# Kernel optimization log

Hardware: AMD Instinct MI355X
Metric: run time of the kernel (lower is better)

The kernel has to match this reference:

```python
import jax, jax.numpy as jnp
import numpy as np

QUERY_LEVELS = jnp.array([300, 500, 900, 1500], dtype=jnp.int32)
MAX_K = 1500
NUM_BOUNDARIES = 3
MAX_OBJECTS = 1500
SCALE = MAX_OBJECTS / NUM_BOUNDARIES * 0.3  # 150.0


def _layernorm(x, g, b, eps=1e-5):
    m = jnp.mean(x, axis=-1, keepdims=True)
    v = jnp.var(x, axis=-1, keepdims=True)
    return (x - m) * jax.lax.rsqrt(v + eps) * g + b


def setup_inputs() -> dict:
    key = jax.random.key(0)
    ks = jax.random.split(key, 14)
    B, C, H, W = 8, 256, 100, 100
    s = 0.02
    return {
        "density_feature": jax.random.normal(ks[0], (B, C, H, W), jnp.float32),
        "encoder_features": jax.random.normal(ks[1], (B, C, H, W), jnp.float32),
        # input_norm (LayerNorm over 2*C)
        "ln_in_g": jnp.ones((2 * C,), jnp.float32),
        "ln_in_b": jnp.zeros((2 * C,), jnp.float32),
        # fc_boundary: Linear(2C->C), Linear(C->3)
        "fcb_w1": jax.random.normal(ks[2], (C, 2 * C), jnp.float32) * s,
        "fcb_b1": jnp.zeros((C,), jnp.float32),
        "fcb_w2": jax.random.normal(ks[3], (NUM_BOUNDARIES, C), jnp.float32) * s,
        "fcb_b2": jnp.full((NUM_BOUNDARIES,), -3.0, jnp.float32),
        "cr_ln_g": jnp.ones((C,), jnp.float32),
        "cr_ln_b": jnp.zeros((C,), jnp.float32),
        "cr_w1": jax.random.normal(ks[4], (C, C), jnp.float32) * s,
        "cr_b1": jnp.zeros((C,), jnp.float32),
        "cr_w2": jax.random.normal(ks[5], (1, C), jnp.float32) * s,
        "cr_b2": jnp.full((1,), 4.0, jnp.float32),
        # channel attention 1x1 convs: C->C//16->C
        "ca_w1": jax.random.normal(ks[6], (C // 16, C), jnp.float32) * s,
        "ca_b1": jnp.zeros((C // 16,), jnp.float32),
        "ca_w2": jax.random.normal(ks[7], (C, C // 16), jnp.float32) * s,
        "ca_b2": jnp.zeros((C,), jnp.float32),
        # spatial attention 7x7 conv, 2->1, no bias
        "sa_w": jax.random.normal(ks[8], (1, 2, 7, 7), jnp.float32) * s,
        # spatial_weight_conv 1x1, C->1
        "sw_w": jax.random.normal(ks[9], (1, C), jnp.float32) * s,
        "sw_b": jnp.zeros((1,), jnp.float32),
    }


def reference(density_feature, encoder_features, ln_in_g, ln_in_b,
              fcb_w1, fcb_b1, fcb_w2, fcb_b2,
              cr_ln_g, cr_ln_b, cr_w1, cr_b1, cr_w2, cr_b2,
              ca_w1, ca_b1, ca_w2, ca_b2, sa_w, sw_w, sw_b):
    B, C, H, W = density_feature.shape
    df = jnp.clip(density_feature, -5.0, 5.0)
    ef = jnp.clip(encoder_features, -5.0, 5.0)

    # ---- boundary prediction from density feature ----
    feat_avg = jnp.mean(df, axis=(2, 3))            # [B, C]
    feat_max = jnp.max(df, axis=(2, 3))             # [B, C]
    gfeat = jnp.concatenate([feat_avg, feat_max], axis=1)  # [B, 2C]
    gfeat = _layernorm(gfeat, ln_in_g, ln_in_b)
    h = jax.nn.relu(gfeat @ fcb_w1.T + fcb_b1)
    raw_boundaries = h @ fcb_w2.T + fcb_b2           # [B, 3]
    # cumulative: b_i = sum_{j<=i} (softplus(raw_j)*SCALE + 5)
    boundaries = jnp.cumsum(jax.nn.softplus(raw_boundaries) * SCALE + 5.0, axis=1)

    cr = _layernorm(feat_avg, cr_ln_g, cr_ln_b)
    cr = jax.nn.relu(cr @ cr_w1.T + cr_b1)
    pred_count = jax.nn.softplus(cr @ cr_w2.T + cr_b2)[:, 0]  # [B]

    # ---- num_queries via boundary comparison (eval: N_eval = pred_count) ----
    level = ((pred_count > boundaries[:, 0]).astype(jnp.int32)
             + (pred_count > boundaries[:, 1]).astype(jnp.int32)
             + (pred_count > boundaries[:, 2]).astype(jnp.int32))
    num_queries = QUERY_LEVELS[level]

    # ---- CBAM channel attention ----
    x = ef
    gap = jnp.mean(x, axis=(2, 3))                   # [B, C]
    ca = jax.nn.relu(gap @ ca_w1.T + ca_b1)
    ca = jax.nn.sigmoid(ca @ ca_w2.T + ca_b2)        # [B, C]
    x = x * ca[:, :, None, None]

    # ---- CBAM spatial attention ----
    sa_avg = jnp.mean(x, axis=1, keepdims=True)      # [B,1,H,W]
    sa_max = jnp.max(x, axis=1, keepdims=True)
    sa = jnp.concatenate([sa_avg, sa_max], axis=1)   # [B,2,H,W]
    sa = jax.lax.conv_general_dilated(sa, sa_w, (1, 1), [(3, 3), (3, 3)],
                                      dimension_numbers=("NCHW", "OIHW", "NCHW"))
    x = x * jax.nn.sigmoid(sa)

    # ---- spatial weight map + topk reference points ----
    wmap = jax.nn.sigmoid(jnp.einsum("bchw,oc->bohw", x, sw_w) + sw_b[None, :, None, None])
    spatial_weight_map = wmap.reshape(B, 1, H * W)
    weight_flat = wmap.reshape(B, H * W)
    actual_k = min(H * W, MAX_K)
    _, topk_ind = jax.lax.top_k(weight_flat, actual_k)   # [B, k]
    topk_y = ((topk_ind // W).astype(jnp.float32) + 0.5) / H
    topk_x = ((topk_ind % W).astype(jnp.float32) + 0.5) / W
    ref_points = jnp.stack([topk_x, topk_y], axis=-1)    # [B,k,2]
    ref_points = jnp.concatenate([ref_points, jnp.full_like(ref_points, 0.05)], axis=-1)
    if actual_k < MAX_K:
        pad = jnp.zeros((B, MAX_K - actual_k, 4), ref_points.dtype)
        ref_points = jnp.concatenate([ref_points, pad], axis=1)

    return (boundaries, raw_boundaries, pred_count, num_queries,
            spatial_weight_map, ref_points)
```

## Files before the change

kernel.cpp:

```cpp
#include <hip/hip_runtime.h>
#include <cstdint>
#include <cstddef>

#define BB 8
#define CC 256
#define HH 100
#define WW 100
#define HW 10000
#define KTOP 1500
#define QB 64

#define WS_AVG   0
#define WS_MAX   2048
#define WS_GAP   4096
#define WS_CA    6144
#define WS_CASW  8192
#define WS_SW    10240
#define WS_SAVG  90240
#define WS_SMAX  170240
#define WS_SEL   250240
#define WS_AK    250248

#define O_BND 0
#define O_RAW 24
#define O_CNT 48
#define O_NQ  56
#define O_WMAP 64
#define O_REF 80064

__device__ __forceinline__ float clip5(float v){ return fminf(fmaxf(v, -5.f), 5.f); }
__device__ __forceinline__ float softplusf(float x){ return fmaxf(x, 0.f) + log1pf(expf(-fabsf(x))); }
__device__ __forceinline__ float sigmoidf(float x){ return 1.f / (1.f + expf(-x)); }

__device__ __forceinline__ float wsum(float v){
#pragma unroll
  for (int o = 32; o; o >>= 1) v += __shfl_down(v, o, 64);
  return v;
}
__device__ __forceinline__ float wmaxr(float v){
#pragma unroll
  for (int o = 32; o; o >>= 1) v = fmaxf(v, __shfl_down(v, o, 64));
  return v;
}

__device__ __forceinline__ float bsum256(float v, volatile float* red){
  v = wsum(v);
  int w = threadIdx.x >> 6;
  if ((threadIdx.x & 63) == 0) red[w] = v;
  __syncthreads();
  float r = (red[0] + red[1]) + (red[2] + red[3]);
  __syncthreads();
  return r;
}

__device__ __forceinline__ void acc1(const float4& v, float& s, float& m){
  float a = clip5(v.x), b = clip5(v.y), c = clip5(v.z), d = clip5(v.w);
  s += (a + b) + (c + d);
  m = fmaxf(m, fmaxf(fmaxf(a, b), fmaxf(c, d)));
}

__global__ __launch_bounds__(256) void k_reduce(const float* __restrict__ df,
                                                const float* __restrict__ ef,
                                                float* __restrict__ ws){
  int gw = blockIdx.x * 4 + (threadIdx.x >> 6);
  bool isDf = gw < 2048;
  int bc = isDf ? gw : gw - 2048;
  int lane = threadIdx.x & 63;
  const float4* __restrict__ src =
      reinterpret_cast<const float4*>((isDf ? df : ef) + (size_t)bc * HW);

  float s = 0.f, m = -1e30f;
  float4 A[8], Bv[8];

#pragma unroll
  for (int j = 0; j < 8; j++) A[j]  = src[64 * j + lane];
#pragma unroll
  for (int j = 0; j < 8; j++) Bv[j] = src[512 + 64 * j + lane];
#pragma unroll
  for (int j = 0; j < 8; j++) acc1(A[j], s, m);
#pragma unroll
  for (int j = 0; j < 8; j++) A[j]  = src[1024 + 64 * j + lane];
#pragma unroll
  for (int j = 0; j < 8; j++) acc1(Bv[j], s, m);
#pragma unroll
  for (int j = 0; j < 8; j++) Bv[j] = src[1536 + 64 * j + lane];
#pragma unroll
  for (int j = 0; j < 8; j++) acc1(A[j], s, m);
#pragma unroll
  for (int j = 0; j < 7; j++) A[j]  = src[2048 + 64 * j + lane];
  A[7] = src[(2496 + lane < 2500) ? (2496 + lane) : lane];
#pragma unroll
  for (int j = 0; j < 8; j++) acc1(Bv[j], s, m);
#pragma unroll
  for (int j = 0; j < 7; j++) acc1(A[j], s, m);
  if (lane < 4) acc1(A[7], s, m);

  s = wsum(s); m = wmaxr(m);
  if (lane == 0){
    if (isDf){ ws[WS_AVG + bc] = s * (1.f / HW); ws[WS_MAX + bc] = m; }
    else      { ws[WS_GAP + bc] = s * (1.f / HW); }
  }
}

__global__ __launch_bounds__(256) void k_head(float* __restrict__ ws,
    const float* __restrict__ ln_g, const float* __restrict__ ln_b,
    const float* __restrict__ fw1, const float* __restrict__ fb1,
    const float* __restrict__ fw2, const float* __restrict__ fb2,
    const float* __restrict__ crg, const float* __restrict__ crb,
    const float* __restrict__ cw1, const float* __restrict__ cb1,
    const float* __restrict__ cw2, const float* __restrict__ cb2,
    const float* __restrict__ caw1, const float* __restrict__ cab1,
    const float* __restrict__ caw2, const float* __restrict__ cab2,
    const float* __restrict__ sw_w, float* __restrict__ out){
  int b = blockIdx.x, t = threadIdx.x;
  __shared__ float red[4];
  __shared__ __align__(16) float gl[512];
  __shared__ __align__(16) float hl[256];
  __shared__ float rawl[3];
  __shared__ float bnd[3];
  __shared__ __align__(16) float al[16];

  float fa = ws[WS_AVG + b * CC + t];
  float fm = ws[WS_MAX + b * CC + t];

  float s  = bsum256(fa + fm, red);
  float s2 = bsum256(fa * fa + fm * fm, red);
  float mean = s * (1.f / 512.f);
  float var  = s2 * (1.f / 512.f) - mean * mean;
  float inv  = rsqrtf(var + 1e-5f);
  gl[t]       = (fa - mean) * inv * ln_g[t]       + ln_b[t];
  gl[t + 256] = (fm - mean) * inv * ln_g[t + 256] + ln_b[t + 256];
  __syncthreads();

  {
    const float4* __restrict__ glv = reinterpret_cast<const float4*>(gl);
    const float4* __restrict__ w1v = reinterpret_cast<const float4*>(fw1 + t * 512);
    float acc = fb1[t];
#pragma unroll 8
    for (int k = 0; k < 128; k++){
      float4 g = glv[k], w = w1v[k];
      acc += g.x * w.x + g.y * w.y + g.z * w.z + g.w * w.w;
    }
    hl[t] = fmaxf(acc, 0.f);
  }
  __syncthreads();
  if (t < 3){
    const float4* __restrict__ hv  = reinterpret_cast<const float4*>(hl);
    const float4* __restrict__ w2v = reinterpret_cast<const float4*>(fw2 + t * 256);
    float r = fb2[t];
#pragma unroll 8
    for (int k = 0; k < 64; k++){
      float4 h = hv[k], w = w2v[k];
      r += h.x * w.x + h.y * w.y + h.z * w.z + h.w * w.w;
    }
    rawl[t] = r;
  }
  __syncthreads();
  if (t == 0){
    float cum = 0.f;
    for (int o = 0; o < 3; o++){
      float rv = rawl[o];
      out[O_RAW + b * 3 + o] = rv;
      cum += softplusf(rv) * 150.f + 5.f;
      out[O_BND + b * 3 + o] = cum;
      bnd[o] = cum;
    }
  }
  __syncthreads();

  float sc  = bsum256(fa, red);
  float sc2 = bsum256(fa * fa, red);
  float m2 = sc * (1.f / 256.f);
  float v2 = sc2 * (1.f / 256.f) - m2 * m2;
  float inv2 = rsqrtf(v2 + 1e-5f);
  hl[t] = (fa - m2) * inv2 * crg[t] + crb[t];
  __syncthreads();
  float h2;
  {
    const float4* __restrict__ hv  = reinterpret_cast<const float4*>(hl);
    const float4* __restrict__ w1v = reinterpret_cast<const float4*>(cw1 + t * 256);
    float acc2 = cb1[t];
#pragma unroll 8
    for (int k = 0; k < 64; k++){
      float4 h = hv[k], w = w1v[k];
      acc2 += h.x * w.x + h.y * w.y + h.z * w.z + h.w * w.w;
    }
    h2 = fmaxf(acc2, 0.f);
  }
  float pv = bsum256(h2 * cw2[t], red);
  if (t == 0){
    float pred = softplusf(pv + cb2[0]);
    out[O_CNT + b] = pred;
    int lvl = (pred > bnd[0]) + (pred > bnd[1]) + (pred > bnd[2]);
    const float QL[4] = {300.f, 500.f, 900.f, 1500.f};
    out[O_NQ + b] = QL[lvl];
  }

  float gp = ws[WS_GAP + b * CC + t];
  __syncthreads();
  hl[t] = gp;
  __syncthreads();
  if (t < 16){
    const float4* __restrict__ hv  = reinterpret_cast<const float4*>(hl);
    const float4* __restrict__ w1v = reinterpret_cast<const float4*>(caw1 + t * 256);
    float a = cab1[t];
#pragma unroll 8
    for (int k = 0; k < 64; k++){
      float4 h = hv[k], w = w1v[k];
      a += h.x * w.x + h.y * w.y + h.z * w.z + h.w * w.w;
    }
    al[t] = fmaxf(a, 0.f);
  }
  __syncthreads();
  float a2 = cab2[t];
  {
    const float4* __restrict__ av  = reinterpret_cast<const float4*>(al);
    const float4* __restrict__ w2v = reinterpret_cast<const float4*>(caw2 + t * 16);
#pragma unroll
    for (int k = 0; k < 4; k++){
      float4 h = av[k], w = w2v[k];
      a2 += h.x * w.x + h.y * w.y + h.z * w.z + h.w * w.w;
    }
  }
  float cav = sigmoidf(a2);
  ws[WS_CA + b * CC + t]   = cav;
  ws[WS_CASW + b * CC + t] = cav * sw_w[t];
}

__device__ __forceinline__ void px_acc(const float4& v, float ca, float cs,
                                       float4& sum, float4& mx, float4& sw){
  float a = clip5(v.x), b = clip5(v.y), c = clip5(v.z), d = clip5(v.w);
  sum.x += a * ca; sum.y += b * ca; sum.z += c * ca; sum.w += d * ca;
  mx.x = fmaxf(mx.x, a * ca); mx.y = fmaxf(mx.y, b * ca);
  mx.z = fmaxf(mx.z, c * ca); mx.w = fmaxf(mx.w, d * ca);
  sw.x = fmaf(a, cs, sw.x); sw.y = fmaf(b, cs, sw.y);
  sw.z = fmaf(c, cs, sw.z); sw.w = fmaf(d, cs, sw.w);
}

__global__ __launch_bounds__(256) void k_pixel(const float* __restrict__ ef,
                                               float* __restrict__ ws){
  int b = blockIdx.y;
  int t = threadIdx.x;
  int w = t >> 6, lane = t & 63;
  __shared__ float caL[256], cswL[256];
  __shared__ float4 part[3][4][QB];
  caL[t]  = ws[WS_CA + b * CC + t];
  cswL[t] = ws[WS_CASW + b * CC + t];
  __syncthreads();

  int q = blockIdx.x * QB + lane;
  const size_t st = HW / 4;
  size_t off = (q < (int)st) ? (size_t)q : 0;
  const float4* __restrict__ base =
      reinterpret_cast<const float4*>(ef + (size_t)b * CC * HW) + off;
  int c0 = w * 64;

  float4 sum = {0.f, 0.f, 0.f, 0.f};
  float4 mx  = {-1e30f, -1e30f, -1e30f, -1e30f};
  float4 sw  = {0.f, 0.f, 0.f, 0.f};

  float4 A[8], Bv[8];
#pragma unroll
  for (int j = 0; j < 8; j++) A[j] = base[(size_t)(c0 + j) * st];
#pragma unroll
  for (int s = 0; s < 4; s++){
    int cA = c0 + (2 * s) * 8;
    int cB = c0 + (2 * s + 1) * 8;
#pragma unroll
    for (int j = 0; j < 8; j++) Bv[j] = base[(size_t)(cB + j) * st];
#pragma unroll
    for (int j = 0; j < 8; j++) px_acc(A[j], caL[cA + j], cswL[cA + j], sum, mx, sw);
    if (s < 3){
      int cN = c0 + (2 * s + 2) * 8;
#pragma unroll
      for (int j = 0; j < 8; j++) A[j] = base[(size_t)(cN + j) * st];
    }
#pragma unroll
    for (int j = 0; j < 8; j++) px_acc(Bv[j], caL[cB + j], cswL[cB + j], sum, mx, sw);
  }

  part[0][w][lane] = sum;
  part[1][w][lane] = mx;
  part[2][w][lane] = sw;
  __syncthreads();
  if (t < QB){
    float4 S = part[0][0][t], M = part[1][0][t], W4 = part[2][0][t];
#pragma unroll
    for (int wv = 1; wv < 4; wv++){
      float4 s1 = part[0][wv][t], m1 = part[1][wv][t], w1 = part[2][wv][t];
      S.x += s1.x; S.y += s1.y; S.z += s1.z; S.w += s1.w;
      M.x = fmaxf(M.x, m1.x); M.y = fmaxf(M.y, m1.y);
      M.z = fmaxf(M.z, m1.z); M.w = fmaxf(M.w, m1.w);
      W4.x += w1.x; W4.y += w1.y; W4.z += w1.z; W4.w += w1.w;
    }
    int q2 = blockIdx.x * QB + t;
    if (q2 < (int)st){
      float4 avg = {S.x * (1.f / 256.f), S.y * (1.f / 256.f),
                    S.z * (1.f / 256.f), S.w * (1.f / 256.f)};
      reinterpret_cast<float4*>(ws + WS_SAVG + (size_t)b * HW)[q2] = avg;
      reinterpret_cast<float4*>(ws + WS_SMAX + (size_t)b * HW)[q2] = M;
      reinterpret_cast<float4*>(ws + WS_SW   + (size_t)b * HW)[q2] = W4;
    }
  }
}

__global__ __launch_bounds__(256) void k_conv(const float* __restrict__ ws,
                                              const float* __restrict__ sa_w,
                                              const float* __restrict__ sw_b,
                                              float* __restrict__ out){
  __shared__ float wc[98];
  if (threadIdx.x < 98) wc[threadIdx.x] = sa_w[threadIdx.x];
  __syncthreads();
  int b = blockIdx.y;
  int p = blockIdx.x * 256 + threadIdx.x;
  if (p >= HW) return;
  int h = p / WW, w = p - h * WW;
  const float* s0 = ws + WS_SAVG + (size_t)b * HW;
  const float* s1 = ws + WS_SMAX + (size_t)b * HW;
  float acc = 0.f;
#pragma unroll
  for (int kh = 0; kh < 7; kh++){
    int hy = h + kh - 3;
    if (hy < 0 || hy >= HH) continue;
#pragma unroll
    for (int kw = 0; kw < 7; kw++){
      int wx = w + kw - 3;
      if (wx < 0 || wx >= WW) continue;
      int q = hy * WW + wx;
      acc += s0[q] * wc[kh * 7 + kw] + s1[q] * wc[49 + kh * 7 + kw];
    }
  }
  float wm = sigmoidf(ws[WS_SW + (size_t)b * HW + p] * sigmoidf(acc) + sw_b[0]);
  out[O_WMAP + (size_t)b * HW + p] = wm;
}

__global__ __launch_bounds__(1024) void k_select(const float* __restrict__ outw,
                                                 float* __restrict__ ws,
                                                 float* __restrict__ out){
  __shared__ unsigned long long red64[16];
  __shared__ unsigned red32[16];
  __shared__ unsigned slo, shi, sbc;
  __shared__ unsigned acnt, runbase;
  int b = blockIdx.x, t = threadIdx.x;
  int w = t >> 6, lane = t & 63;

  const float* src = outw + O_WMAP + (size_t)b * HW;
  unsigned rv[10];
#pragma unroll
  for (int j = 0; j < 10; j++){
    int i = t + j * 1024;
    rv[j] = (i < HW) ? __float_as_uint(src[i]) : 0u;
  }

  unsigned lo = 0u, hi = 0xFFFFFFFFu;
  while (lo < hi){
    unsigned span = hi - lo;
    unsigned q1 = lo + (span >> 2);
    unsigned q2 = lo + (span >> 1);
    unsigned q3 = lo + span - (span >> 2);
    unsigned long long pk = 0;
#pragma unroll
    for (int j = 0; j < 10; j++){
      unsigned v = rv[j];
      pk += (unsigned long long)(v > q1)
          + ((unsigned long long)(v > q2) << 16)
          + ((unsigned long long)(v > q3) << 32);
    }
#pragma unroll
    for (int o = 32; o; o >>= 1) pk += __shfl_down(pk, o, 64);
    if (lane == 0) red64[w] = pk;
    __syncthreads();
    if (t == 0){
      unsigned long long tot = 0;
#pragma unroll
      for (int q = 0; q < 16; q++) tot += red64[q];
      unsigned c1 = (unsigned)(tot & 0xFFFFu);
      unsigned c2 = (unsigned)((tot >> 16) & 0xFFFFu);
      unsigned c3 = (unsigned)((tot >> 32) & 0xFFFFu);
      unsigned nlo, nhi;
      if (c1 < (unsigned)KTOP)      { nlo = lo;      nhi = q1; }
      else if (c2 < (unsigned)KTOP) { nlo = q1 + 1u; nhi = q2; }
      else if (c3 < (unsigned)KTOP) { nlo = q2 + 1u; nhi = q3; }
      else                          { nlo = q3 + 1u; nhi = hi; }
      slo = nlo; shi = nhi;
    }
    __syncthreads();
    lo = slo; hi = shi;
    __syncthreads();
  }
  unsigned vthr = lo;

  {
    unsigned c = 0;
#pragma unroll
    for (int j = 0; j < 10; j++) c += (rv[j] > vthr) ? 1u : 0u;
#pragma unroll
    for (int o = 32; o; o >>= 1) c += __shfl_down((int)c, o, 64);
    if (lane == 0) red32[w] = c;
    __syncthreads();
    if (t == 0){
      unsigned tot = 0;
#pragma unroll
      for (int q = 0; q < 16; q++) tot += red32[q];
      sbc = tot;
      acnt = 0; runbase = 0;
    }
    __syncthreads();
  }
  unsigned nabove = sbc;
  int neq = KTOP - (int)nabove;
  if (t == 0) reinterpret_cast<int*>(ws)[WS_SEL + b] = (int)nabove;

  unsigned long long* AK = reinterpret_cast<unsigned long long*>(ws + WS_AK) + (size_t)b * KTOP;
#pragma unroll
  for (int j = 0; j < 10; j++){
    int i = t + j * 1024;
    bool p = (i < HW) && (rv[j] > vthr);
    unsigned long long m = __ballot(p);
    unsigned base = 0;
    if (lane == 0 && m) base = atomicAdd(&acnt, (unsigned)__popcll(m));
    base = (unsigned)__shfl((int)base, 0, 64);
    if (p){
      unsigned pos = base + (unsigned)__popcll(m & ((1ull << lane) - 1ull));
      AK[pos] = ((unsigned long long)rv[j] << 32) | (unsigned long long)(0xFFFFFFFFu - (unsigned)i);
    }
  }

  for (int j = 0; j < 10; j++){
    int i = j * 1024 + t;
    bool eq = (i < HW) && (rv[j] == vthr);
    unsigned long long bal = __ballot(eq);
    if (lane == 0) red32[w] = (unsigned)__popcll(bal);
    __syncthreads();
    unsigned pre = runbase;
    for (int q = 0; q < w; q++) pre += red32[q];
    unsigned myr = pre + (unsigned)__popcll(bal & ((1ull << lane) - 1ull));
    if (eq && myr < (unsigned)neq){
      int pos = (int)nabove + (int)myr;
      float y = ((float)(i / WW) + 0.5f) * (1.f / HH);
      float x = ((float)(i % WW) + 0.5f) * (1.f / WW);
      float* rp = out + O_REF + ((size_t)b * KTOP + pos) * 4;
      rp[0] = x; rp[1] = y; rp[2] = 0.05f; rp[3] = 0.05f;
    }
    __syncthreads();
    if (t == 0){
      unsigned tot = 0;
#pragma unroll
      for (int q = 0; q < 16; q++) tot += red32[q];
      runbase += tot;
    }
    __syncthreads();
    if (runbase >= (unsigned)neq) break;
  }
}

__global__ __launch_bounds__(128) void k_rank(const float* __restrict__ ws,
                                              float* __restrict__ out){
  int b = blockIdx.x, chunk = blockIdx.y, t = threadIdx.x;
  int nA = reinterpret_cast<const int*>(ws)[WS_SEL + b];
  __shared__ unsigned long long K[KTOP];
  const unsigned long long* AK =
      reinterpret_cast<const unsigned long long*>(ws + WS_AK) + (size_t)b * KTOP;
  for (int i = t; i < nA; i += 128) K[i] = AK[i];
  __syncthreads();
  int i = chunk * 128 + t;
  if (i >= nA) return;
  unsigned long long Ki = K[i];
  int r = 0;
  for (int j = 0; j < nA; j++) r += (K[j] > Ki);
  unsigned idx = 0xFFFFFFFFu - (unsigned)(Ki & 0xFFFFFFFFull);
  float y = ((float)(idx / WW) + 0.5f) * (1.f / HH);
  float x = ((float)(idx % WW) + 0.5f) * (1.f / WW);
  float* rp = out + O_REF + ((size_t)b * KTOP + r) * 4;
  rp[0] = x; rp[1] = y; rp[2] = 0.05f; rp[3] = 0.05f;
}

extern "C" void kernel_launch(void* const* d_in, const int* in_sizes, int n_in,
                              void* d_out, int out_size, void* d_ws, size_t ws_size,
                              hipStream_t stream) {
  const float* df   = (const float*)d_in[0];
  const float* ef   = (const float*)d_in[1];
  const float* ln_g = (const float*)d_in[2];
  const float* ln_b = (const float*)d_in[3];
  const float* fw1  = (const float*)d_in[4];
  const float* fb1  = (const float*)d_in[5];
  const float* fw2  = (const float*)d_in[6];
  const float* fb2  = (const float*)d_in[7];
  const float* crg  = (const float*)d_in[8];
  const float* crb  = (const float*)d_in[9];
  const float* cw1  = (const float*)d_in[10];
  const float* cb1  = (const float*)d_in[11];
  const float* cw2  = (const float*)d_in[12];
  const float* cb2  = (const float*)d_in[13];
  const float* caw1 = (const float*)d_in[14];
  const float* cab1 = (const float*)d_in[15];
  const float* caw2 = (const float*)d_in[16];
  const float* cab2 = (const float*)d_in[17];
  const float* sa_w = (const float*)d_in[18];
  const float* sw_w = (const float*)d_in[19];
  const float* sw_b = (const float*)d_in[20];
  float* out = (float*)d_out;
  float* ws  = (float*)d_ws;

  k_reduce<<<1024, 256, 0, stream>>>(df, ef, ws);
  k_head<<<8, 256, 0, stream>>>(ws, ln_g, ln_b, fw1, fb1, fw2, fb2,
                                crg, crb, cw1, cb1, cw2, cb2,
                                caw1, cab1, caw2, cab2, sw_w, out);
  k_pixel<<<dim3(40, 8), 256, 0, stream>>>(ef, ws);
  k_conv<<<dim3(40, 8), 256, 0, stream>>>(ws, sa_w, sw_b, out);
  k_select<<<8, 1024, 0, stream>>>(out, ws, out);
  k_rank<<<dim3(8, 12), 128, 0, stream>>>(ws, out);
}
```

Measured before the change: 146.7 us.

## Split reduce rows across two waves and pixel channels across four blocks

k_reduce now assigns each (b,c) row to two wavefronts that each cover half the row, then merges the halves through shared memory, so twice as many blocks are launched. k_pixel gains a z grid dimension that splits the 256 channels into four 64-channel groups. Each group writes partial sum/max/weighted-sum planes to new workspace regions, and a new k_comb kernel merges them and applies the average scaling. The aim is more parallelism and better latency hiding on a memory-bound pass, in exchange for an extra kernel launch and extra workspace traffic for the partial planes.

```diff
diff --git a/kernel.cpp b/kernel.cpp
--- a/kernel.cpp
+++ b/kernel.cpp
@@ -20,6 +20,8 @@
 #define WS_SMAX  170240
 #define WS_SEL   250240
 #define WS_AK    250248
+#define WS_P1    274256
+#define PSET     240000
 
 #define O_BND 0
 #define O_RAW 24
@@ -62,43 +64,44 @@
 __global__ __launch_bounds__(256) void k_reduce(const float* __restrict__ df,
                                                 const float* __restrict__ ef,
                                                 float* __restrict__ ws){
-  int gw = blockIdx.x * 4 + (threadIdx.x >> 6);
-  bool isDf = gw < 2048;
-  int bc = isDf ? gw : gw - 2048;
-  int lane = threadIdx.x & 63;
+  int t = threadIdx.x;
+  int w = t >> 6, lane = t & 63;
+  int row = blockIdx.x * 2 + (w >> 1);
+  int half = w & 1;
+  bool isDf = row < 2048;
+  int bc = isDf ? row : row - 2048;
   const float4* __restrict__ src =
-      reinterpret_cast<const float4*>((isDf ? df : ef) + (size_t)bc * HW);
-
+      reinterpret_cast<const float4*>((isDf ? df : ef) + (size_t)bc * HW) + half * 1250;
+
+  float4 A[8], Bv[8], C[4];
+#pragma unroll
+  for (int j = 0; j < 8; j++) A[j]  = src[j * 64 + lane];
+#pragma unroll
+  for (int j = 0; j < 8; j++) Bv[j] = src[512 + j * 64 + lane];
   float s = 0.f, m = -1e30f;
-  float4 A[8], Bv[8];
-
-#pragma unroll
-  for (int j = 0; j < 8; j++) A[j]  = src[64 * j + lane];
-#pragma unroll
-  for (int j = 0; j < 8; j++) Bv[j] = src[512 + 64 * j + lane];
 #pragma unroll
   for (int j = 0; j < 8; j++) acc1(A[j], s, m);
 #pragma unroll
-  for (int j = 0; j < 8; j++) A[j]  = src[1024 + 64 * j + lane];
+  for (int j = 0; j < 3; j++) C[j] = src[1024 + j * 64 + lane];
+  C[3] = src[(1216 + lane < 1250) ? (1216 + lane) : lane];
 #pragma unroll
   for (int j = 0; j < 8; j++) acc1(Bv[j], s, m);
 #pragma unroll
-  for (int j = 0; j < 8; j++) Bv[j] = src[1536 + 64 * j + lane];
-#pragma unroll
-  for (int j = 0; j < 8; j++) acc1(A[j], s, m);
-#pragma unroll
-  for (int j = 0; j < 7; j++) A[j]  = src[2048 + 64 * j + lane];
-  A[7] = src[(2496 + lane < 2500) ? (2496 + lane) : lane];
-#pragma unroll
-  for (int j = 0; j < 8; j++) acc1(Bv[j], s, m);
-#pragma unroll
-  for (int j = 0; j < 7; j++) acc1(A[j], s, m);
-  if (lane < 4) acc1(A[7], s, m);
+  for (int j = 0; j < 3; j++) acc1(C[j], s, m);
+  if (lane < 34) acc1(C[3], s, m);
 
   s = wsum(s); m = wmaxr(m);
-  if (lane == 0){
-    if (isDf){ ws[WS_AVG + bc] = s * (1.f / HW); ws[WS_MAX + bc] = m; }
-    else      { ws[WS_GAP + bc] = s * (1.f / HW); }
+  __shared__ float rs[4], rm[4];
+  if (lane == 0){ rs[w] = s; rm[w] = m; }
+  __syncthreads();
+  if (t < 2){
+    int r2 = blockIdx.x * 2 + t;
+    bool d2 = r2 < 2048;
+    int bc2 = d2 ? r2 : r2 - 2048;
+    float S = rs[2 * t] + rs[2 * t + 1];
+    float M = fmaxf(rm[2 * t], rm[2 * t + 1]);
+    if (d2){ ws[WS_AVG + bc2] = S * (1.f / HW); ws[WS_MAX + bc2] = M; }
+    else     ws[WS_GAP + bc2] = S * (1.f / HW);
   }
 }
 
@@ -239,7 +242,7 @@
 
 __global__ __launch_bounds__(256) void k_pixel(const float* __restrict__ ef,
                                                float* __restrict__ ws){
-  int b = blockIdx.y;
+  int b = blockIdx.y, z = blockIdx.z;
   int t = threadIdx.x;
   int w = t >> 6, lane = t & 63;
   __shared__ float caL[256], cswL[256];
@@ -253,7 +256,7 @@
   size_t off = (q < (int)st) ? (size_t)q : 0;
   const float4* __restrict__ base =
       reinterpret_cast<const float4*>(ef + (size_t)b * CC * HW) + off;
-  int c0 = w * 64;
+  int c0 = z * 64 + w * 16;
 
   float4 sum = {0.f, 0.f, 0.f, 0.f};
   float4 mx  = {-1e30f, -1e30f, -1e30f, -1e30f};
@@ -261,23 +264,13 @@
 
   float4 A[8], Bv[8];
 #pragma unroll
-  for (int j = 0; j < 8; j++) A[j] = base[(size_t)(c0 + j) * st];
-#pragma unroll
-  for (int s = 0; s < 4; s++){
-    int cA = c0 + (2 * s) * 8;
-    int cB = c0 + (2 * s + 1) * 8;
-#pragma unroll
-    for (int j = 0; j < 8; j++) Bv[j] = base[(size_t)(cB + j) * st];
-#pragma unroll
-    for (int j = 0; j < 8; j++) px_acc(A[j], caL[cA + j], cswL[cA + j], sum, mx, sw);
-    if (s < 3){
-      int cN = c0 + (2 * s + 2) * 8;
-#pragma unroll
-      for (int j = 0; j < 8; j++) A[j] = base[(size_t)(cN + j) * st];
-    }
-#pragma unroll
-    for (int j = 0; j < 8; j++) px_acc(Bv[j], caL[cB + j], cswL[cB + j], sum, mx, sw);
-  }
+  for (int j = 0; j < 8; j++) A[j]  = base[(size_t)(c0 + j) * st];
+#pragma unroll
+  for (int j = 0; j < 8; j++) Bv[j] = base[(size_t)(c0 + 8 + j) * st];
+#pragma unroll
+  for (int j = 0; j < 8; j++) px_acc(A[j],  caL[c0 + j],     cswL[c0 + j],     sum, mx, sw);
+#pragma unroll
+  for (int j = 0; j < 8; j++) px_acc(Bv[j], caL[c0 + 8 + j], cswL[c0 + 8 + j], sum, mx, sw);
 
   part[0][w][lane] = sum;
   part[1][w][lane] = mx;
@@ -295,13 +288,48 @@
     }
     int q2 = blockIdx.x * QB + t;
     if (q2 < (int)st){
-      float4 avg = {S.x * (1.f / 256.f), S.y * (1.f / 256.f),
-                    S.z * (1.f / 256.f), S.w * (1.f / 256.f)};
-      reinterpret_cast<float4*>(ws + WS_SAVG + (size_t)b * HW)[q2] = avg;
-      reinterpret_cast<float4*>(ws + WS_SMAX + (size_t)b * HW)[q2] = M;
-      reinterpret_cast<float4*>(ws + WS_SW   + (size_t)b * HW)[q2] = W4;
-    }
-  }
+      size_t fo = (size_t)b * HW;
+      float4* Sd; float4* Md; float4* Wd;
+      if (z == 0){
+        Sd = reinterpret_cast<float4*>(ws + WS_SAVG + fo);
+        Md = reinterpret_cast<float4*>(ws + WS_SMAX + fo);
+        Wd = reinterpret_cast<float4*>(ws + WS_SW   + fo);
+      } else {
+        float* p = ws + WS_P1 + (size_t)(z - 1) * PSET;
+        Sd = reinterpret_cast<float4*>(p + fo);
+        Md = reinterpret_cast<float4*>(p + 80000 + fo);
+        Wd = reinterpret_cast<float4*>(p + 160000 + fo);
+      }
+      Sd[q2] = S;
+      Md[q2] = M;
+      Wd[q2] = W4;
+    }
+  }
+}
+
+__global__ __launch_bounds__(256) void k_comb(float* __restrict__ ws){
+  int gid = blockIdx.x * 256 + threadIdx.x;
+  if (gid >= BB * 2500) return;
+  int b = gid / 2500, q = gid - b * 2500;
+  size_t fo = (size_t)b * HW;
+  float4* S = reinterpret_cast<float4*>(ws + WS_SAVG + fo);
+  float4* M = reinterpret_cast<float4*>(ws + WS_SMAX + fo);
+  float4* W = reinterpret_cast<float4*>(ws + WS_SW   + fo);
+  float4 s = S[q], m = M[q], w = W[q];
+#pragma unroll
+  for (int k = 0; k < 3; k++){
+    float* p = ws + WS_P1 + (size_t)k * PSET;
+    float4 s1 = reinterpret_cast<const float4*>(p + fo)[q];
+    float4 m1 = reinterpret_cast<const float4*>(p + 80000 + fo)[q];
+    float4 w1 = reinterpret_cast<const float4*>(p + 160000 + fo)[q];
+    s.x += s1.x; s.y += s1.y; s.z += s1.z; s.w += s1.w;
+    m.x = fmaxf(m.x, m1.x); m.y = fmaxf(m.y, m1.y);
+    m.z = fmaxf(m.z, m1.z); m.w = fmaxf(m.w, m1.w);
+    w.x += w1.x; w.y += w1.y; w.z += w1.z; w.w += w1.w;
+  }
+  float4 avg = {s.x * (1.f / 256.f), s.y * (1.f / 256.f),
+                s.z * (1.f / 256.f), s.w * (1.f / 256.f)};
+  S[q] = avg; M[q] = m; W[q] = w;
 }
 
 __global__ __launch_bounds__(256) void k_conv(const float* __restrict__ ws,
@@ -502,11 +530,12 @@
   float* out = (float*)d_out;
   float* ws  = (float*)d_ws;
 
-  k_reduce<<<1024, 256, 0, stream>>>(df, ef, ws);
+  k_reduce<<<2048, 256, 0, stream>>>(df, ef, ws);
   k_head<<<8, 256, 0, stream>>>(ws, ln_g, ln_b, fw1, fb1, fw2, fb2,
                                 crg, crb, cw1, cb1, cw2, cb2,
                                 caw1, cab1, caw2, cab2, sw_w, out);
-  k_pixel<<<dim3(40, 8), 256, 0, stream>>>(ef, ws);
+  k_pixel<<<dim3(40, 8, 4), 256, 0, stream>>>(ef, ws);
+  k_comb<<<(BB * 2500 + 255) / 256, 256, 0, stream>>>(ws);
   k_conv<<<dim3(40, 8), 256, 0, stream>>>(ws, sa_w, sw_b, out);
   k_select<<<8, 1024, 0, stream>>>(out, ws, out);
   k_rank<<<dim3(8, 12), 128, 0, stream>>>(ws, out);
```

New measurement: 149.4 us. Within noise of the previous version (+1.8%).

## Fuse spatial conv into top-k select kernel and streamline threshold search

Applied to the files above, without the earlier changes.

Merges the 7x7 spatial-attention conv plus sigmoid weight-map kernel into the top-k selection kernel, so each of 8 blocks computes its weight map in registers without a separate launch or a reload from global memory. The radix-style threshold search now starts from an upper bound of 1.0 (sigmoid outputs are in [0,1]), which cuts iterations. It also replaces the single-thread reduction with a wave-shuffle reduction on double-buffered shared slots, removing one barrier per iteration. The risk is that the conv now runs on only 8 workgroups instead of 320, which loses parallelism for that stage.

```diff
diff --git a/kernel.cpp b/kernel.cpp
--- a/kernel.cpp
+++ b/kernel.cpp
@@ -304,55 +304,52 @@
   }
 }
 
-__global__ __launch_bounds__(256) void k_conv(const float* __restrict__ ws,
-                                              const float* __restrict__ sa_w,
-                                              const float* __restrict__ sw_b,
-                                              float* __restrict__ out){
+__global__ __launch_bounds__(1024) void k_tail(float* __restrict__ ws,
+                                               const float* __restrict__ sa_w,
+                                               const float* __restrict__ sw_b,
+                                               float* __restrict__ out){
   __shared__ float wc[98];
-  if (threadIdx.x < 98) wc[threadIdx.x] = sa_w[threadIdx.x];
-  __syncthreads();
-  int b = blockIdx.y;
-  int p = blockIdx.x * 256 + threadIdx.x;
-  if (p >= HW) return;
-  int h = p / WW, w = p - h * WW;
-  const float* s0 = ws + WS_SAVG + (size_t)b * HW;
-  const float* s1 = ws + WS_SMAX + (size_t)b * HW;
-  float acc = 0.f;
-#pragma unroll
-  for (int kh = 0; kh < 7; kh++){
-    int hy = h + kh - 3;
-    if (hy < 0 || hy >= HH) continue;
-#pragma unroll
-    for (int kw = 0; kw < 7; kw++){
-      int wx = w + kw - 3;
-      if (wx < 0 || wx >= WW) continue;
-      int q = hy * WW + wx;
-      acc += s0[q] * wc[kh * 7 + kw] + s1[q] * wc[49 + kh * 7 + kw];
-    }
-  }
-  float wm = sigmoidf(ws[WS_SW + (size_t)b * HW + p] * sigmoidf(acc) + sw_b[0]);
-  out[O_WMAP + (size_t)b * HW + p] = wm;
-}
-
-__global__ __launch_bounds__(1024) void k_select(const float* __restrict__ outw,
-                                                 float* __restrict__ ws,
-                                                 float* __restrict__ out){
-  __shared__ unsigned long long red64[16];
+  __shared__ unsigned long long red64[2][16];
   __shared__ unsigned red32[16];
-  __shared__ unsigned slo, shi, sbc;
   __shared__ unsigned acnt, runbase;
   int b = blockIdx.x, t = threadIdx.x;
   int w = t >> 6, lane = t & 63;
-
-  const float* src = outw + O_WMAP + (size_t)b * HW;
+  if (t < 98) wc[t] = sa_w[t];
+  if (t == 0){ acnt = 0; runbase = 0; }
+  __syncthreads();
+
+  const float* s0 = ws + WS_SAVG + (size_t)b * HW;
+  const float* s1 = ws + WS_SMAX + (size_t)b * HW;
+  const float* sww = ws + WS_SW + (size_t)b * HW;
+  float swb = sw_b[0];
+
   unsigned rv[10];
 #pragma unroll
   for (int j = 0; j < 10; j++){
-    int i = t + j * 1024;
-    rv[j] = (i < HW) ? __float_as_uint(src[i]) : 0u;
-  }
-
-  unsigned lo = 0u, hi = 0xFFFFFFFFu;
+    int i = j * 1024 + t;
+    if (i < HW){
+      int h = i / WW, x = i - h * WW;
+      float acc = 0.f;
+#pragma unroll
+      for (int kh = 0; kh < 7; kh++){
+        int hy = h + kh - 3;
+        if (hy < 0 || hy >= HH) continue;
+#pragma unroll
+        for (int kw = 0; kw < 7; kw++){
+          int wx = x + kw - 3;
+          if (wx < 0 || wx >= WW) continue;
+          int q = hy * WW + wx;
+          acc += s0[q] * wc[kh * 7 + kw] + s1[q] * wc[49 + kh * 7 + kw];
+        }
+      }
+      float wm = sigmoidf(sww[i] * sigmoidf(acc) + swb);
+      out[O_WMAP + (size_t)b * HW + i] = wm;
+      rv[j] = __float_as_uint(wm);
+    } else rv[j] = 0u;
+  }
+
+  unsigned lo = 0u, hi = 0x3F800000u;
+  int par = 0;
   while (lo < hi){
     unsigned span = hi - lo;
     unsigned q1 = lo + (span >> 2);
@@ -368,53 +365,44 @@
     }
 #pragma unroll
     for (int o = 32; o; o >>= 1) pk += __shfl_down(pk, o, 64);
-    if (lane == 0) red64[w] = pk;
+    if (lane == 0) red64[par][w] = pk;
     __syncthreads();
-    if (t == 0){
-      unsigned long long tot = 0;
-#pragma unroll
-      for (int q = 0; q < 16; q++) tot += red64[q];
-      unsigned c1 = (unsigned)(tot & 0xFFFFu);
-      unsigned c2 = (unsigned)((tot >> 16) & 0xFFFFu);
-      unsigned c3 = (unsigned)((tot >> 32) & 0xFFFFu);
-      unsigned nlo, nhi;
-      if (c1 < (unsigned)KTOP)      { nlo = lo;      nhi = q1; }
-      else if (c2 < (unsigned)KTOP) { nlo = q1 + 1u; nhi = q2; }
-      else if (c3 < (unsigned)KTOP) { nlo = q2 + 1u; nhi = q3; }
-      else                          { nlo = q3 + 1u; nhi = hi; }
-      slo = nlo; shi = nhi;
-    }
+    unsigned long long v16 = (lane < 16) ? red64[par][lane] : 0ull;
+#pragma unroll
+    for (int o = 8; o; o >>= 1) v16 += __shfl_down(v16, o, 64);
+    unsigned long long tot = __shfl(v16, 0, 64);
+    unsigned c1 = (unsigned)(tot & 0xFFFFu);
+    unsigned c2 = (unsigned)((tot >> 16) & 0xFFFFu);
+    unsigned c3 = (unsigned)((tot >> 32) & 0xFFFFu);
+    if (c1 < (unsigned)KTOP)      hi = q1;
+    else if (c2 < (unsigned)KTOP){ lo = q1 + 1u; hi = q2; }
+    else if (c3 < (unsigned)KTOP){ lo = q2 + 1u; hi = q3; }
+    else                           lo = q3 + 1u;
+    par ^= 1;
+  }
+  unsigned vthr = lo;
+
+  unsigned nabove;
+  {
+    unsigned long long c = 0;
+#pragma unroll
+    for (int j = 0; j < 10; j++) c += (rv[j] > vthr) ? 1u : 0u;
+#pragma unroll
+    for (int o = 32; o; o >>= 1) c += __shfl_down(c, o, 64);
+    if (lane == 0) red64[par][w] = c;
     __syncthreads();
-    lo = slo; hi = shi;
-    __syncthreads();
-  }
-  unsigned vthr = lo;
-
-  {
-    unsigned c = 0;
-#pragma unroll
-    for (int j = 0; j < 10; j++) c += (rv[j] > vthr) ? 1u : 0u;
-#pragma unroll
-    for (int o = 32; o; o >>= 1) c += __shfl_down((int)c, o, 64);
-    if (lane == 0) red32[w] = c;
-    __syncthreads();
-    if (t == 0){
-      unsigned tot = 0;
-#pragma unroll
-      for (int q = 0; q < 16; q++) tot += red32[q];
-      sbc = tot;
-      acnt = 0; runbase = 0;
-    }
-    __syncthreads();
-  }
-  unsigned nabove = sbc;
+    unsigned long long v16 = (lane < 16) ? red64[par][lane] : 0ull;
+#pragma unroll
+    for (int o = 8; o; o >>= 1) v16 += __shfl_down(v16, o, 64);
+    nabove = (unsigned)__shfl(v16, 0, 64);
+  }
   int neq = KTOP - (int)nabove;
   if (t == 0) reinterpret_cast<int*>(ws)[WS_SEL + b] = (int)nabove;
 
   unsigned long long* AK = reinterpret_cast<unsigned long long*>(ws + WS_AK) + (size_t)b * KTOP;
 #pragma unroll
   for (int j = 0; j < 10; j++){
-    int i = t + j * 1024;
+    int i = j * 1024 + t;
     bool p = (i < HW) && (rv[j] > vthr);
     unsigned long long m = __ballot(p);
     unsigned base = 0;
@@ -507,7 +495,6 @@
                                 crg, crb, cw1, cb1, cw2, cb2,
                                 caw1, cab1, caw2, cab2, sw_w, out);
   k_pixel<<<dim3(40, 8), 256, 0, stream>>>(ef, ws);
-  k_conv<<<dim3(40, 8), 256, 0, stream>>>(ws, sa_w, sw_b, out);
-  k_select<<<8, 1024, 0, stream>>>(out, ws, out);
+  k_tail<<<8, 1024, 0, stream>>>(ws, sa_w, sw_b, out);
   k_rank<<<dim3(8, 12), 128, 0, stream>>>(ws, out);
 }
```

Result: slower. 226.0 us (+54.0%).
